# Optimization experiments

Hardware: AMD Instinct MI355X
Metric: run time of the kernel (lower is better)

Reference implementation:

```python
import jax, jax.numpy as jnp
import numpy as np

D_MODEL, D_K, D_V, N_HEADS = 1024, 64, 64, 16


def setup_inputs() -> dict:
    key = jax.random.key(0)
    ks = jax.random.split(key, 8)
    B, S = 2, 2048
    s = 0.02
    return {
        "x": jax.random.normal(ks[0], (B, S, D_MODEL), dtype=jnp.float32),
        "Wq": jax.random.normal(ks[1], (D_MODEL, N_HEADS * D_K), dtype=jnp.float32) * s,
        "bq": jnp.zeros((N_HEADS * D_K,), dtype=jnp.float32),
        "Wk": jax.random.normal(ks[2], (D_MODEL, N_HEADS * D_K), dtype=jnp.float32) * s,
        "bk": jnp.zeros((N_HEADS * D_K,), dtype=jnp.float32),
        "Wv": jax.random.normal(ks[3], (D_MODEL, N_HEADS * D_V), dtype=jnp.float32) * s,
        "bv": jnp.zeros((N_HEADS * D_V,), dtype=jnp.float32),
        "Wo": jax.random.normal(ks[4], (N_HEADS * D_V, D_MODEL), dtype=jnp.float32) * s,
    }


def reference(x, Wq, bq, Wk, bk, Wv, bv, Wo):
    B, S, _ = x.shape
    split = lambda t, d: t.reshape(B, S, N_HEADS, d).transpose(0, 2, 1, 3)  # [B,H,S,d]
    Q = split(x @ Wq + bq, D_K)
    K = split(x @ Wk + bk, D_K)
    V = split(x @ Wv + bv, D_V)
    scores = jnp.einsum("bhqd,bhkd->bhqk", Q / jnp.sqrt(jnp.float32(D_K)), K)
    # causal mask: x + (1 - 1/tril) == 0 on allowed, -inf on disallowed
    causal = jnp.tril(jnp.ones((S, S), dtype=bool))
    scores = jnp.where(causal, scores, -jnp.inf)
    attn = jax.nn.softmax(scores, axis=-1)
    out = jnp.einsum("bhqk,bhkd->bhqd", attn, V)  # [B,H,S,d_v]
    out = out.transpose(0, 2, 1, 3).reshape(B, S, N_HEADS * D_V)
    return out @ Wo
```

## Files before the change

kernel.cpp:

```cpp
#include <hip/hip_runtime.h>
#include <hip/hip_bf16.h>
#include <hip/hip_fp16.h>
#include <cstdint>

#define DEVINL __device__ __forceinline__

typedef __attribute__((ext_vector_type(4))) float floatx4;
typedef __attribute__((ext_vector_type(8))) __bf16 bf16x8;
typedef __attribute__((ext_vector_type(4))) _Float16 half4;
typedef __attribute__((ext_vector_type(8))) _Float16 half8;
typedef __attribute__((ext_vector_type(4))) unsigned short u16x4;

DEVINL floatx4 mfma_16x16x32(bf16x8 a, bf16x8 b, floatx4 c) {
  return __builtin_amdgcn_mfma_f32_16x16x32_bf16(a, b, c, 0, 0, 0);
}
DEVINL floatx4 mfma_16x16x16_f16(half4 a, half4 b, floatx4 c) {
  return __builtin_amdgcn_mfma_f32_16x16x16f16(a, b, c, 0, 0, 0);
}

DEVINL void async_copy16(const void* g, void* l) {
  __builtin_amdgcn_global_load_lds(
      (__attribute__((address_space(1))) void*)(void*)g,
      (__attribute__((address_space(3))) void*)l, 16, 0, 0);
}

#define QSCALE 0.18033688011112042f

#define VS(d, s) \
  ((d) * 128 + (((((s) >> 3)) ^ ((d) & 7)) << 4) + ((s) & 7) * 2)

__global__ void prep(const float* __restrict__ x, const float* __restrict__ Wq,
                     const float* __restrict__ Wk, const float* __restrict__ Wv,
                     const float* __restrict__ Wo,
                     __hip_bfloat16* __restrict__ xb,
                     __hip_bfloat16* __restrict__ Wt,
                     __hip_bfloat16* __restrict__ Wot) {
  const int z = blockIdx.z;
  const int tx = threadIdx.x, ty = threadIdx.y;
  if (z == 4) {
    const int bi = blockIdx.y * 32 + blockIdx.x;
    const int tid = ty * 32 + tx;
    const int base = bi * 4096 + tid * 4;
#pragma unroll
    for (int j = 0; j < 4; ++j) {
      const int i = base + j * 1024;
      const float4 v = *(const float4*)&x[i];
      xb[i + 0] = __float2bfloat16(v.x);
      xb[i + 1] = __float2bfloat16(v.y);
      xb[i + 2] = __float2bfloat16(v.z);
      xb[i + 3] = __float2bfloat16(v.w);
    }
    return;
  }
  __shared__ float tile[32][33];
  const float* W = (z == 0) ? Wq : (z == 1) ? Wk : (z == 2) ? Wv : Wo;
  __hip_bfloat16* dst = (z < 3) ? (Wt + ((int64_t)z << 20)) : Wot;
  const int k0 = blockIdx.x * 32, n0 = blockIdx.y * 32;
#pragma unroll
  for (int i = 0; i < 32; i += 8)
    tile[ty + i][tx] = W[(int64_t)(k0 + ty + i) * 1024 + n0 + tx];
  __syncthreads();
#pragma unroll
  for (int i = 0; i < 32; i += 8)
    dst[(int64_t)(n0 + ty + i) * 1024 + k0 + tx] =
        __float2bfloat16(tile[tx][ty + i]);
}

template <int MODE, int TM, int TN, int OCC>
__global__ __launch_bounds__(256, OCC) void gemm_bt(
    const __hip_bfloat16* __restrict__ A, const __hip_bfloat16* __restrict__ Bt,
    int M, int N, int K, const float* __restrict__ bq,
    const float* __restrict__ bk, const float* __restrict__ bv,
    __hip_bfloat16* __restrict__ Qb, __hip_bfloat16* __restrict__ Kb,
    _Float16* __restrict__ Vt, float* __restrict__ outf) {
  constexpr int MI = TM / 32, NJ = TN / 32;
  __shared__ __align__(16) char As[TM * 128];
  __shared__ __align__(16) char Bs[TN * 128];
  const int tid = threadIdx.x;
  const int wave = tid >> 6, lane = tid & 63;
  const int quad = lane >> 4, l16 = lane & 15;
  const int bm = blockIdx.x * TM, bn = blockIdx.y * TN;
  const int wm = (wave >> 1) * (TM / 2), wn = (wave & 1) * (TN / 2);
  const int sw = l16 & 7;

  floatx4 acc[MI][NJ] = {};

  for (int k0 = 0; k0 < K; k0 += 64) {
#pragma unroll
    for (int i = 0; i < TM / 32; ++i) {
      const int p = tid + i * 256;
      const int r = p >> 3, cc = (p & 7) ^ (r & 7);
      async_copy16(A + (int64_t)(bm + r) * K + k0 + cc * 8, As + p * 16);
    }
#pragma unroll
    for (int i = 0; i < TN / 32; ++i) {
      const int p = tid + i * 256;
      const int r = p >> 3, cc = (p & 7) ^ (r & 7);
      async_copy16(Bt + (int64_t)(bn + r) * K + k0 + cc * 8, Bs + p * 16);
    }
    __syncthreads();
    bf16x8 af[MI][2], bfr[NJ][2];
#pragma unroll
    for (int i = 0; i < MI; ++i)
#pragma unroll
      for (int h = 0; h < 2; ++h)
        af[i][h] = *(const bf16x8*)(As + (wm + i * 16 + l16) * 128 +
                                    (((h * 4 + quad) ^ sw) << 4));
#pragma unroll
    for (int j = 0; j < NJ; ++j)
#pragma unroll
      for (int h = 0; h < 2; ++h)
        bfr[j][h] = *(const bf16x8*)(Bs + (wn + j * 16 + l16) * 128 +
                                     (((h * 4 + quad) ^ sw) << 4));
#pragma unroll
    for (int i = 0; i < MI; ++i)
#pragma unroll
      for (int j = 0; j < NJ; ++j)
#pragma unroll
        for (int h = 0; h < 2; ++h)
          acc[i][j] = mfma_16x16x32(af[i][h], bfr[j][h], acc[i][j]);
    __syncthreads();
  }

  if (MODE == 1) {
#pragma unroll
    for (int i = 0; i < MI; ++i)
#pragma unroll
      for (int j = 0; j < NJ; ++j) {
        const int n = bn + wn + j * 16 + l16;
#pragma unroll
        for (int r = 0; r < 4; ++r) {
          const int m = bm + wm + i * 16 + quad * 4 + r;
          outf[(int64_t)m * N + n] = acc[i][j][r];
        }
      }
  } else if (bn < 2048) {
#pragma unroll
    for (int i = 0; i < MI; ++i)
#pragma unroll
      for (int j = 0; j < NJ; ++j) {
        const int n = bn + wn + j * 16 + l16;
        const int which = n >> 10, nn = n & 1023;
        const int h = nn >> 6, d = nn & 63;
        const float* bias = (which == 0) ? bq : bk;
#pragma unroll
        for (int r = 0; r < 4; ++r) {
          const int m = bm + wm + i * 16 + quad * 4 + r;
          const int b = m >> 11, s = m & 2047;
          float v = acc[i][j][r] + bias[nn];
          if (which == 0) v *= QSCALE;
          ((which == 0) ? Qb : Kb)[((int64_t)(b * 16 + h) * 2048 + s) * 64 + d] =
              __float2bfloat16(v);
        }
      }
  } else {
    char* scr = (wave & 1) ? Bs : As;
    const int h = ((bn + wn) & 1023) >> 6;
    const int bb = (bm + wm) >> 11;
    const int sbase = (bm + wm) & 2047;
    _Float16* dstV = Vt + (int64_t)(bb * 16 + h) * 64 * 2048;
#pragma unroll
    for (int phase = 0; phase < 2; ++phase) {
      __syncthreads();
      if ((wave >> 1) == phase) {
#pragma unroll
        for (int i = 0; i < 4; ++i)
#pragma unroll
          for (int j = 0; j < 4; ++j) {
            const int d = j * 16 + l16;
#pragma unroll
            for (int r = 0; r < 4; ++r) {
              const int s = i * 16 + quad * 4 + r;
              *(_Float16*)(scr + VS(d, s)) =
                  (_Float16)(acc[i][j][r] + bv[((bn + wn) & 1023) + d]);
            }
          }
      }
      __syncthreads();
      if ((wave >> 1) == phase) {
#pragma unroll
        for (int it = 0; it < 8; ++it) {
          const int idx = lane + it * 64;
          const int d = idx >> 3, sc = idx & 7;
          const half8 vv =
              *(const half8*)(scr + d * 128 + ((sc ^ (d & 7)) << 4));
          *(half8*)(dstV + (int64_t)d * 2048 + sbase + sc * 8) = vv;
        }
      }
    }
  }
}

__global__ __launch_bounds__(256, 3) void attn_kernel(
    const __hip_bfloat16* __restrict__ Qb, const __hip_bfloat16* __restrict__ Kb,
    const _Float16* __restrict__ Vt, __hip_bfloat16* __restrict__ Ab) {
  __shared__ __align__(16) char smem[32768];
  const int tid = threadIdx.x;
  const int wave = tid >> 6, lane = tid & 63;
  const int quad = lane >> 4, l16 = lane & 15;
  const int c = 31 - (int)(blockIdx.x >> 5);
  const int bh = blockIdx.x & 31;
  const int qbase = c * 64 + wave * 16;
  const int ktmax = c;

  const __hip_bfloat16* Qh = Qb + (int64_t)bh * 2048 * 64;
  const __hip_bfloat16* Kh = Kb + (int64_t)bh * 2048 * 64;
  const _Float16* Vh = Vt + (int64_t)bh * 64 * 2048;

  bf16x8 qf[2];
#pragma unroll
  for (int h = 0; h < 2; ++h)
    qf[h] = *(const bf16x8*)&Qh[(int64_t)(qbase + l16) * 64 + h * 32 + quad * 8];

  floatx4 o[4] = {};
  float lsum = 0.f;

  auto stage = [&](int buf, int k0s) {
#pragma unroll
    for (int i = 0; i < 2; ++i) {
      const int p = tid + i * 256;
      const int r = p >> 3, cc = (p & 7) ^ (r & 7);
      async_copy16(Kh + (int64_t)(k0s + r) * 64 + cc * 8,
                   smem + buf * 8192 + p * 16);
      async_copy16(Vh + (int64_t)r * 2048 + k0s + cc * 8,
                   smem + 16384 + buf * 8192 + p * 16);
    }
  };

  stage(0, 0);
  for (int kt = 0; kt <= ktmax; ++kt) {
    const int k0 = kt * 64;
    const int cur = kt & 1;
    __syncthreads();
    if (kt < ktmax) stage(cur ^ 1, k0 + 64);

    const char* kb = smem + cur * 8192;
    const char* vb = smem + 16384 + cur * 8192;
    const int sw = l16 & 7;

    bf16x8 kfr[4][2];
#pragma unroll
    for (int kk = 0; kk < 4; ++kk)
#pragma unroll
      for (int h = 0; h < 2; ++h)
        kfr[kk][h] = *(const bf16x8*)(kb + (kk * 16 + l16) * 128 +
                                      (((h * 4 + quad) ^ sw) << 4));

    floatx4 st[4];
#pragma unroll
    for (int kk = 0; kk < 4; ++kk) {
      floatx4 z = {};
      z = mfma_16x16x32(kfr[kk][0], qf[0], z);
      st[kk] = mfma_16x16x32(kfr[kk][1], qf[1], z);
    }

    half4 vfr[4][4];
#pragma unroll
    for (int dt = 0; dt < 4; ++dt)
#pragma unroll
      for (int kk = 0; kk < 4; ++kk)
        vfr[dt][kk] = *(const half4*)(vb + (dt * 16 + l16) * 128 +
                                      (((kk * 2 + (quad >> 1)) ^ sw) << 4) +
                                      (quad & 1) * 8);

    const bool masked = (kt == ktmax);
    half4 pf[4];
#pragma unroll
    for (int kk = 0; kk < 4; ++kk) {
#pragma unroll
      for (int r = 0; r < 4; ++r) {
        const int key = k0 + kk * 16 + quad * 4 + r;
        float p = __builtin_amdgcn_exp2f(st[kk][r]);
        if (masked && key > qbase + l16) p = 0.f;
        lsum += p;
        pf[kk][r] = (_Float16)p;
      }
    }

#pragma unroll
    for (int dt = 0; dt < 4; ++dt)
#pragma unroll
      for (int kk = 0; kk < 4; ++kk)
        o[dt] = mfma_16x16x16_f16(vfr[dt][kk], pf[kk], o[dt]);
  }

  lsum += __shfl_xor(lsum, 16, 64);
  lsum += __shfl_xor(lsum, 32, 64);
  const float invl = 1.0f / lsum;

  const int b = bh >> 4, h = bh & 15;
#pragma unroll
  for (int dt = 0; dt < 4; ++dt) {
    u16x4 pack;
#pragma unroll
    for (int r = 0; r < 4; ++r)
      pack[r] = __builtin_bit_cast(unsigned short,
                                   __float2bfloat16(o[dt][r] * invl));
    *(u16x4*)&Ab[(int64_t)(b * 2048 + qbase + l16) * 1024 + h * 64 + dt * 16 +
                 quad * 4] = pack;
  }
}

extern "C" void kernel_launch(void* const* d_in, const int* in_sizes, int n_in,
                              void* d_out, int out_size, void* d_ws,
                              size_t ws_size, hipStream_t stream) {
  const float* x = (const float*)d_in[0];
  const float* Wq = (const float*)d_in[1];
  const float* bq = (const float*)d_in[2];
  const float* Wk = (const float*)d_in[3];
  const float* bk = (const float*)d_in[4];
  const float* Wv = (const float*)d_in[5];
  const float* bv = (const float*)d_in[6];
  const float* Wo = (const float*)d_in[7];
  float* out = (float*)d_out;

  char* ws = (char*)d_ws;
  __hip_bfloat16* xb = (__hip_bfloat16*)(ws);
  __hip_bfloat16* Wt = (__hip_bfloat16*)(ws + (8ll << 20));
  __hip_bfloat16* Wot = (__hip_bfloat16*)(ws + (14ll << 20));
  __hip_bfloat16* Qb = (__hip_bfloat16*)(ws + (16ll << 20));
  __hip_bfloat16* Kb = (__hip_bfloat16*)(ws + (24ll << 20));
  _Float16* Vt = (_Float16*)(ws + (32ll << 20));
  __hip_bfloat16* Ab = xb;

  prep<<<dim3(32, 32, 5), dim3(32, 8), 0, stream>>>(x, Wq, Wk, Wv, Wo, xb, Wt,
                                                    Wot);
  gemm_bt<0, 128, 128, 3><<<dim3(32, 24), 256, 0, stream>>>(
      xb, Wt, 4096, 3072, 1024, bq, bk, bv, Qb, Kb, Vt, nullptr);
  attn_kernel<<<dim3(1024), 256, 0, stream>>>(Qb, Kb, Vt, Ab);
  gemm_bt<1, 128, 64, 2><<<dim3(32, 16), 256, 0, stream>>>(
      Ab, Wot, 4096, 1024, 1024, nullptr, nullptr, nullptr, nullptr, nullptr,
      nullptr, out);
}
```

Before: 168.8 us.

## Pair high and low causal query tiles per attention block for load balance

Each attention block now handles two query tiles, one near the end of the sequence and its mirror near the start, so every block walks the same number of key tiles and the causal triangle is evenly balanced. K/V tiles staged in shared memory are reused for both query tiles while the low tile is still active, and the grid is halved to 512 blocks. Register pressure rises from the doubled accumulators and launch bounds drop to 2 blocks per SM, which lowers occupancy. Fewer blocks also means less parallelism to hide latency.

```diff
diff --git a/kernel.cpp b/kernel.cpp
--- a/kernel.cpp
+++ b/kernel.cpp
@@ -191,29 +191,33 @@
   }
 }
 
-__global__ __launch_bounds__(256, 3) void attn_kernel(
+__global__ __launch_bounds__(256, 2) void attn_kernel(
     const __hip_bfloat16* __restrict__ Qb, const __hip_bfloat16* __restrict__ Kb,
     const _Float16* __restrict__ Vt, __hip_bfloat16* __restrict__ Ab) {
   __shared__ __align__(16) char smem[32768];
   const int tid = threadIdx.x;
   const int wave = tid >> 6, lane = tid & 63;
   const int quad = lane >> 4, l16 = lane & 15;
-  const int c = 31 - (int)(blockIdx.x >> 5);
+  const int pr = (int)(blockIdx.x >> 5);
   const int bh = blockIdx.x & 31;
-  const int qbase = c * 64 + wave * 16;
-  const int ktmax = c;
+  const int cH = 31 - pr, cL = pr;
+  const int qH = cH * 64 + wave * 16;
+  const int qL = cL * 64 + wave * 16;
+  const int ktmax = cH;
 
   const __hip_bfloat16* Qh = Qb + (int64_t)bh * 2048 * 64;
   const __hip_bfloat16* Kh = Kb + (int64_t)bh * 2048 * 64;
   const _Float16* Vh = Vt + (int64_t)bh * 64 * 2048;
 
-  bf16x8 qf[2];
-#pragma unroll
-  for (int h = 0; h < 2; ++h)
-    qf[h] = *(const bf16x8*)&Qh[(int64_t)(qbase + l16) * 64 + h * 32 + quad * 8];
-
-  floatx4 o[4] = {};
-  float lsum = 0.f;
+  bf16x8 qfH[2], qfL[2];
+#pragma unroll
+  for (int h = 0; h < 2; ++h) {
+    qfH[h] = *(const bf16x8*)&Qh[(int64_t)(qH + l16) * 64 + h * 32 + quad * 8];
+    qfL[h] = *(const bf16x8*)&Qh[(int64_t)(qL + l16) * 64 + h * 32 + quad * 8];
+  }
+
+  floatx4 oH[4] = {}, oL[4] = {};
+  float lsH = 0.f, lsL = 0.f;
 
   auto stage = [&](int buf, int k0s) {
 #pragma unroll
@@ -237,6 +241,7 @@
     const char* kb = smem + cur * 8192;
     const char* vb = smem + 16384 + cur * 8192;
     const int sw = l16 & 7;
+    const bool doL = (kt <= cL);
 
     bf16x8 kfr[4][2];
 #pragma unroll
@@ -246,12 +251,20 @@
         kfr[kk][h] = *(const bf16x8*)(kb + (kk * 16 + l16) * 128 +
                                       (((h * 4 + quad) ^ sw) << 4));
 
-    floatx4 st[4];
+    floatx4 stH[4], stL[4];
 #pragma unroll
     for (int kk = 0; kk < 4; ++kk) {
       floatx4 z = {};
-      z = mfma_16x16x32(kfr[kk][0], qf[0], z);
-      st[kk] = mfma_16x16x32(kfr[kk][1], qf[1], z);
+      z = mfma_16x16x32(kfr[kk][0], qfH[0], z);
+      stH[kk] = mfma_16x16x32(kfr[kk][1], qfH[1], z);
+    }
+    if (doL) {
+#pragma unroll
+      for (int kk = 0; kk < 4; ++kk) {
+        floatx4 z = {};
+        z = mfma_16x16x32(kfr[kk][0], qfL[0], z);
+        stL[kk] = mfma_16x16x32(kfr[kk][1], qfL[1], z);
+      }
     }
 
     half4 vfr[4][4];
@@ -263,41 +276,70 @@
                                       (((kk * 2 + (quad >> 1)) ^ sw) << 4) +
                                       (quad & 1) * 8);
 
-    const bool masked = (kt == ktmax);
-    half4 pf[4];
-#pragma unroll
-    for (int kk = 0; kk < 4; ++kk) {
-#pragma unroll
-      for (int r = 0; r < 4; ++r) {
-        const int key = k0 + kk * 16 + quad * 4 + r;
-        float p = __builtin_amdgcn_exp2f(st[kk][r]);
-        if (masked && key > qbase + l16) p = 0.f;
-        lsum += p;
-        pf[kk][r] = (_Float16)p;
-      }
-    }
-
-#pragma unroll
-    for (int dt = 0; dt < 4; ++dt)
-#pragma unroll
-      for (int kk = 0; kk < 4; ++kk)
-        o[dt] = mfma_16x16x16_f16(vfr[dt][kk], pf[kk], o[dt]);
-  }
-
-  lsum += __shfl_xor(lsum, 16, 64);
-  lsum += __shfl_xor(lsum, 32, 64);
-  const float invl = 1.0f / lsum;
+    {
+      const bool masked = (kt == cH);
+      half4 pf[4];
+#pragma unroll
+      for (int kk = 0; kk < 4; ++kk) {
+#pragma unroll
+        for (int r = 0; r < 4; ++r) {
+          const int key = k0 + kk * 16 + quad * 4 + r;
+          float p = __builtin_amdgcn_exp2f(stH[kk][r]);
+          if (masked && key > qH + l16) p = 0.f;
+          lsH += p;
+          pf[kk][r] = (_Float16)p;
+        }
+      }
+#pragma unroll
+      for (int dt = 0; dt < 4; ++dt)
+#pragma unroll
+        for (int kk = 0; kk < 4; ++kk)
+          oH[dt] = mfma_16x16x16_f16(vfr[dt][kk], pf[kk], oH[dt]);
+    }
+    if (doL) {
+      const bool masked = (kt == cL);
+      half4 pf[4];
+#pragma unroll
+      for (int kk = 0; kk < 4; ++kk) {
+#pragma unroll
+        for (int r = 0; r < 4; ++r) {
+          const int key = k0 + kk * 16 + quad * 4 + r;
+          float p = __builtin_amdgcn_exp2f(stL[kk][r]);
+          if (masked && key > qL + l16) p = 0.f;
+          lsL += p;
+          pf[kk][r] = (_Float16)p;
+        }
+      }
+#pragma unroll
+      for (int dt = 0; dt < 4; ++dt)
+#pragma unroll
+        for (int kk = 0; kk < 4; ++kk)
+          oL[dt] = mfma_16x16x16_f16(vfr[dt][kk], pf[kk], oL[dt]);
+    }
+  }
+
+  lsH += __shfl_xor(lsH, 16, 64);
+  lsH += __shfl_xor(lsH, 32, 64);
+  lsL += __shfl_xor(lsL, 16, 64);
+  lsL += __shfl_xor(lsL, 32, 64);
+  const float invH = 1.0f / lsH;
+  const float invL = 1.0f / lsL;
 
   const int b = bh >> 4, h = bh & 15;
 #pragma unroll
   for (int dt = 0; dt < 4; ++dt) {
-    u16x4 pack;
-#pragma unroll
-    for (int r = 0; r < 4; ++r)
-      pack[r] = __builtin_bit_cast(unsigned short,
-                                   __float2bfloat16(o[dt][r] * invl));
-    *(u16x4*)&Ab[(int64_t)(b * 2048 + qbase + l16) * 1024 + h * 64 + dt * 16 +
-                 quad * 4] = pack;
+    u16x4 packH, packL;
+#pragma unroll
+    for (int r = 0; r < 4; ++r) {
+      packH[r] = __builtin_bit_cast(unsigned short,
+                                    __float2bfloat16(oH[dt][r] * invH));
+      packL[r] = __builtin_bit_cast(unsigned short,
+                                    __float2bfloat16(oL[dt][r] * invL));
+    }
+    *(u16x4*)&Ab[(int64_t)(b * 2048 + qH + l16) * 1024 + h * 64 + dt * 16 +
+                 quad * 4] = packH;
+    *(u16x4*)&Ab[(int64_t)(b * 2048 + qL + l16) * 1024 + h * 64 + dt * 16 +
+                 quad * 4] = packL;
   }
 }
 
@@ -327,7 +369,7 @@
                                                     Wot);
   gemm_bt<0, 128, 128, 3><<<dim3(32, 24), 256, 0, stream>>>(
       xb, Wt, 4096, 3072, 1024, bq, bk, bv, Qb, Kb, Vt, nullptr);
-  attn_kernel<<<dim3(1024), 256, 0, stream>>>(Qb, Kb, Vt, Ab);
+  attn_kernel<<<dim3(512), 256, 0, stream>>>(Qb, Kb, Vt, Ab);
   gemm_bt<1, 128, 64, 2><<<dim3(32, 16), 256, 0, stream>>>(
       Ab, Wot, 4096, 1024, 1024, nullptr, nullptr, nullptr, nullptr, nullptr,
       nullptr, out);
```

Measured after the change: 167.7 us. No clear change (-0.7%).

## Split attention key tiles across waves with LDS cross-wave reduction

Applied to the files above, without the earlier changes.

The attention kernel stops having each wave own 16 query rows and stream every key tile through double-buffered shared memory. Each wave now handles all 64 query rows of the block for a strided subset of key tiles, reading K and V fragments straight from global memory. Partial outputs and row sums are then combined through a larger LDS buffer at the end. This is meant to drop the per-tile barriers and async staging and to balance work across waves, at the cost of more accumulator registers, lower occupancy (launch bound lowered from 3 to 2), uncoalesced global fragment loads, and an extra reduction pass.

```diff
diff --git a/kernel.cpp b/kernel.cpp
--- a/kernel.cpp
+++ b/kernel.cpp
@@ -191,113 +191,114 @@
   }
 }
 
-__global__ __launch_bounds__(256, 3) void attn_kernel(
+__global__ __launch_bounds__(256, 2) void attn_kernel(
     const __hip_bfloat16* __restrict__ Qb, const __hip_bfloat16* __restrict__ Kb,
     const _Float16* __restrict__ Vt, __hip_bfloat16* __restrict__ Ab) {
-  __shared__ __align__(16) char smem[32768];
+  __shared__ __align__(16) char smem[69632];
   const int tid = threadIdx.x;
   const int wave = tid >> 6, lane = tid & 63;
   const int quad = lane >> 4, l16 = lane & 15;
   const int c = 31 - (int)(blockIdx.x >> 5);
   const int bh = blockIdx.x & 31;
-  const int qbase = c * 64 + wave * 16;
-  const int ktmax = c;
+  const int qbase = c * 64;
 
   const __hip_bfloat16* Qh = Qb + (int64_t)bh * 2048 * 64;
   const __hip_bfloat16* Kh = Kb + (int64_t)bh * 2048 * 64;
   const _Float16* Vh = Vt + (int64_t)bh * 64 * 2048;
 
-  bf16x8 qf[2];
-#pragma unroll
-  for (int h = 0; h < 2; ++h)
-    qf[h] = *(const bf16x8*)&Qh[(int64_t)(qbase + l16) * 64 + h * 32 + quad * 8];
-
-  floatx4 o[4] = {};
-  float lsum = 0.f;
-
-  auto stage = [&](int buf, int k0s) {
-#pragma unroll
-    for (int i = 0; i < 2; ++i) {
-      const int p = tid + i * 256;
-      const int r = p >> 3, cc = (p & 7) ^ (r & 7);
-      async_copy16(Kh + (int64_t)(k0s + r) * 64 + cc * 8,
-                   smem + buf * 8192 + p * 16);
-      async_copy16(Vh + (int64_t)r * 2048 + k0s + cc * 8,
-                   smem + 16384 + buf * 8192 + p * 16);
-    }
-  };
-
-  stage(0, 0);
-  for (int kt = 0; kt <= ktmax; ++kt) {
+  bf16x8 qf[4][2];
+#pragma unroll
+  for (int qc = 0; qc < 4; ++qc)
+#pragma unroll
+    for (int h = 0; h < 2; ++h)
+      qf[qc][h] = *(const bf16x8*)&Qh[(int64_t)(qbase + qc * 16 + l16) * 64 +
+                                      h * 32 + quad * 8];
+
+  floatx4 o[4][4] = {};
+  float ls[4] = {};
+
+  for (int kt = wave; kt <= c; kt += 4) {
     const int k0 = kt * 64;
-    const int cur = kt & 1;
-    __syncthreads();
-    if (kt < ktmax) stage(cur ^ 1, k0 + 64);
-
-    const char* kb = smem + cur * 8192;
-    const char* vb = smem + 16384 + cur * 8192;
-    const int sw = l16 & 7;
-
     bf16x8 kfr[4][2];
 #pragma unroll
     for (int kk = 0; kk < 4; ++kk)
 #pragma unroll
       for (int h = 0; h < 2; ++h)
-        kfr[kk][h] = *(const bf16x8*)(kb + (kk * 16 + l16) * 128 +
-                                      (((h * 4 + quad) ^ sw) << 4));
-
-    floatx4 st[4];
-#pragma unroll
-    for (int kk = 0; kk < 4; ++kk) {
-      floatx4 z = {};
-      z = mfma_16x16x32(kfr[kk][0], qf[0], z);
-      st[kk] = mfma_16x16x32(kfr[kk][1], qf[1], z);
-    }
-
+        kfr[kk][h] = *(const bf16x8*)&Kh[(int64_t)(k0 + kk * 16 + l16) * 64 +
+                                         h * 32 + quad * 8];
     half4 vfr[4][4];
 #pragma unroll
     for (int dt = 0; dt < 4; ++dt)
 #pragma unroll
       for (int kk = 0; kk < 4; ++kk)
-        vfr[dt][kk] = *(const half4*)(vb + (dt * 16 + l16) * 128 +
-                                      (((kk * 2 + (quad >> 1)) ^ sw) << 4) +
-                                      (quad & 1) * 8);
-
-    const bool masked = (kt == ktmax);
-    half4 pf[4];
-#pragma unroll
-    for (int kk = 0; kk < 4; ++kk) {
-#pragma unroll
-      for (int r = 0; r < 4; ++r) {
-        const int key = k0 + kk * 16 + quad * 4 + r;
-        float p = __builtin_amdgcn_exp2f(st[kk][r]);
-        if (masked && key > qbase + l16) p = 0.f;
-        lsum += p;
-        pf[kk][r] = (_Float16)p;
-      }
-    }
-
+        vfr[dt][kk] = *(const half4*)&Vh[(int64_t)(dt * 16 + l16) * 2048 + k0 +
+                                         kk * 16 + quad * 4];
+
+    const bool diag = (kt == c);
+#pragma unroll
+    for (int qc = 0; qc < 4; ++qc) {
+      floatx4 st[4];
+#pragma unroll
+      for (int kk = 0; kk < 4; ++kk) {
+        floatx4 z = {};
+        z = mfma_16x16x32(kfr[kk][0], qf[qc][0], z);
+        st[kk] = mfma_16x16x32(kfr[kk][1], qf[qc][1], z);
+      }
+      half4 pf[4];
+#pragma unroll
+      for (int kk = 0; kk < 4; ++kk) {
+#pragma unroll
+        for (int r = 0; r < 4; ++r) {
+          const int key = k0 + kk * 16 + quad * 4 + r;
+          float p = __builtin_amdgcn_exp2f(st[kk][r]);
+          if (diag && key > qbase + qc * 16 + l16) p = 0.f;
+          ls[qc] += p;
+          pf[kk][r] = (_Float16)p;
+        }
+      }
+#pragma unroll
+      for (int dt = 0; dt < 4; ++dt)
+#pragma unroll
+        for (int kk = 0; kk < 4; ++kk)
+          o[dt][qc] = mfma_16x16x16_f16(vfr[dt][kk], pf[kk], o[dt][qc]);
+    }
+  }
+
+  {
+    char* ob = smem + wave * 17408;
 #pragma unroll
     for (int dt = 0; dt < 4; ++dt)
 #pragma unroll
-      for (int kk = 0; kk < 4; ++kk)
-        o[dt] = mfma_16x16x16_f16(vfr[dt][kk], pf[kk], o[dt]);
-  }
-
-  lsum += __shfl_xor(lsum, 16, 64);
-  lsum += __shfl_xor(lsum, 32, 64);
-  const float invl = 1.0f / lsum;
-
+      for (int qc = 0; qc < 4; ++qc)
+        *(floatx4*)(ob + (dt * 4 + qc) * 1024 + lane * 16) = o[dt][qc];
+    float* lsb = (float*)(ob + 16384);
+#pragma unroll
+    for (int qc = 0; qc < 4; ++qc) lsb[qc * 64 + lane] = ls[qc];
+  }
+  __syncthreads();
+
+  const int dt = wave;
   const int b = bh >> 4, h = bh & 15;
 #pragma unroll
-  for (int dt = 0; dt < 4; ++dt) {
+  for (int qc = 0; qc < 4; ++qc) {
+    floatx4 s = {};
+    float lt = 0.f;
+#pragma unroll
+    for (int w = 0; w < 4; ++w) {
+      s += *(const floatx4*)(smem + w * 17408 + (dt * 4 + qc) * 1024 +
+                             lane * 16);
+      lt += ((const float*)(smem + w * 17408 + 16384))[qc * 64 + lane];
+    }
+    lt += __shfl_xor(lt, 16, 64);
+    lt += __shfl_xor(lt, 32, 64);
+    const float inv = 1.0f / lt;
     u16x4 pack;
 #pragma unroll
     for (int r = 0; r < 4; ++r)
       pack[r] = __builtin_bit_cast(unsigned short,
-                                   __float2bfloat16(o[dt][r] * invl));
-    *(u16x4*)&Ab[(int64_t)(b * 2048 + qbase + l16) * 1024 + h * 64 + dt * 16 +
-                 quad * 4] = pack;
+                                   __float2bfloat16(s[r] * inv));
+    *(u16x4*)&Ab[(int64_t)(b * 2048 + qbase + qc * 16 + l16) * 1024 + h * 64 +
+                 dt * 16 + quad * 4] = pack;
   }
 }
 
```

Result: slower. 191.0 us (+13.1%).

## Split attention key loop across two wave groups with shared-memory reduction

Applied to the files above, without the earlier changes.

Doubles the attention block to 512 threads: two groups of four waves each process alternating 64-key tiles for the same 64 queries, each with its own double-buffered LDS region. At the end, group 1 writes its partial output and row sums to shared memory and group 0 combines them and writes the normalized result. This is meant to halve the serial key-loop length per block, which matters most for the long causal rows. In exchange it doubles LDS per block, adds a reduction step and a sync, and lowers the occupancy bound.

```diff
diff --git a/kernel.cpp b/kernel.cpp
--- a/kernel.cpp
+++ b/kernel.cpp
@@ -191,17 +191,19 @@
   }
 }
 
-__global__ __launch_bounds__(256, 3) void attn_kernel(
+__global__ __launch_bounds__(512, 2) void attn_kernel(
     const __hip_bfloat16* __restrict__ Qb, const __hip_bfloat16* __restrict__ Kb,
     const _Float16* __restrict__ Vt, __hip_bfloat16* __restrict__ Ab) {
-  __shared__ __align__(16) char smem[32768];
+  __shared__ __align__(16) char smem[65536];
   const int tid = threadIdx.x;
   const int wave = tid >> 6, lane = tid & 63;
+  const int g = wave >> 2;
+  const int w4 = wave & 3;
+  const int gtid = w4 * 64 + lane;
   const int quad = lane >> 4, l16 = lane & 15;
   const int c = 31 - (int)(blockIdx.x >> 5);
   const int bh = blockIdx.x & 31;
-  const int qbase = c * 64 + wave * 16;
-  const int ktmax = c;
+  const int qbase = c * 64 + w4 * 16;
 
   const __hip_bfloat16* Qh = Qb + (int64_t)bh * 2048 * 64;
   const __hip_bfloat16* Kh = Kb + (int64_t)bh * 2048 * 64;
@@ -215,89 +217,108 @@
   floatx4 o[4] = {};
   float lsum = 0.f;
 
+  char* const gb = smem + g * 32768;
+
   auto stage = [&](int buf, int k0s) {
 #pragma unroll
     for (int i = 0; i < 2; ++i) {
-      const int p = tid + i * 256;
+      const int p = gtid + i * 256;
       const int r = p >> 3, cc = (p & 7) ^ (r & 7);
       async_copy16(Kh + (int64_t)(k0s + r) * 64 + cc * 8,
-                   smem + buf * 8192 + p * 16);
+                   gb + buf * 16384 + p * 16);
       async_copy16(Vh + (int64_t)r * 2048 + k0s + cc * 8,
-                   smem + 16384 + buf * 8192 + p * 16);
+                   gb + buf * 16384 + 8192 + p * 16);
     }
   };
 
-  stage(0, 0);
-  for (int kt = 0; kt <= ktmax; ++kt) {
-    const int k0 = kt * 64;
-    const int cur = kt & 1;
+  const int NT = (c >> 1) + 1;
+  if (g <= c) stage(0, g * 64);
+
+  for (int t = 0; t < NT; ++t) {
+    const int kt = 2 * t + g;
+    const bool active = (kt <= c);
     __syncthreads();
-    if (kt < ktmax) stage(cur ^ 1, k0 + 64);
-
-    const char* kb = smem + cur * 8192;
-    const char* vb = smem + 16384 + cur * 8192;
-    const int sw = l16 & 7;
-
-    bf16x8 kfr[4][2];
-#pragma unroll
-    for (int kk = 0; kk < 4; ++kk)
-#pragma unroll
-      for (int h = 0; h < 2; ++h)
-        kfr[kk][h] = *(const bf16x8*)(kb + (kk * 16 + l16) * 128 +
-                                      (((h * 4 + quad) ^ sw) << 4));
-
-    floatx4 st[4];
-#pragma unroll
-    for (int kk = 0; kk < 4; ++kk) {
-      floatx4 z = {};
-      z = mfma_16x16x32(kfr[kk][0], qf[0], z);
-      st[kk] = mfma_16x16x32(kfr[kk][1], qf[1], z);
-    }
-
-    half4 vfr[4][4];
+    if (active && kt + 2 <= c) stage((t + 1) & 1, (kt + 2) * 64);
+    if (active) {
+      const int k0 = kt * 64;
+      const char* kb = gb + (t & 1) * 16384;
+      const char* vb = kb + 8192;
+      const int sw = l16 & 7;
+
+      bf16x8 kfr[4][2];
+#pragma unroll
+      for (int kk = 0; kk < 4; ++kk)
+#pragma unroll
+        for (int h = 0; h < 2; ++h)
+          kfr[kk][h] = *(const bf16x8*)(kb + (kk * 16 + l16) * 128 +
+                                        (((h * 4 + quad) ^ sw) << 4));
+
+      floatx4 st[4];
+#pragma unroll
+      for (int kk = 0; kk < 4; ++kk) {
+        floatx4 z = {};
+        z = mfma_16x16x32(kfr[kk][0], qf[0], z);
+        st[kk] = mfma_16x16x32(kfr[kk][1], qf[1], z);
+      }
+
+      half4 vfr[4][4];
+#pragma unroll
+      for (int dt = 0; dt < 4; ++dt)
+#pragma unroll
+        for (int kk = 0; kk < 4; ++kk)
+          vfr[dt][kk] = *(const half4*)(vb + (dt * 16 + l16) * 128 +
+                                        (((kk * 2 + (quad >> 1)) ^ sw) << 4) +
+                                        (quad & 1) * 8);
+
+      const bool masked = (kt == c);
+      half4 pf[4];
+#pragma unroll
+      for (int kk = 0; kk < 4; ++kk) {
+#pragma unroll
+        for (int r = 0; r < 4; ++r) {
+          const int key = k0 + kk * 16 + quad * 4 + r;
+          float p = __builtin_amdgcn_exp2f(st[kk][r]);
+          if (masked && key > qbase + l16) p = 0.f;
+          lsum += p;
+          pf[kk][r] = (_Float16)p;
+        }
+      }
+
+#pragma unroll
+      for (int dt = 0; dt < 4; ++dt)
+#pragma unroll
+        for (int kk = 0; kk < 4; ++kk)
+          o[dt] = mfma_16x16x16_f16(vfr[dt][kk], pf[kk], o[dt]);
+    }
+  }
+
+  __syncthreads();
+  if (g == 1) {
+    char* ob = smem + w4 * 4352;
 #pragma unroll
     for (int dt = 0; dt < 4; ++dt)
-#pragma unroll
-      for (int kk = 0; kk < 4; ++kk)
-        vfr[dt][kk] = *(const half4*)(vb + (dt * 16 + l16) * 128 +
-                                      (((kk * 2 + (quad >> 1)) ^ sw) << 4) +
-                                      (quad & 1) * 8);
-
-    const bool masked = (kt == ktmax);
-    half4 pf[4];
-#pragma unroll
-    for (int kk = 0; kk < 4; ++kk) {
-#pragma unroll
-      for (int r = 0; r < 4; ++r) {
-        const int key = k0 + kk * 16 + quad * 4 + r;
-        float p = __builtin_amdgcn_exp2f(st[kk][r]);
-        if (masked && key > qbase + l16) p = 0.f;
-        lsum += p;
-        pf[kk][r] = (_Float16)p;
-      }
-    }
-
-#pragma unroll
-    for (int dt = 0; dt < 4; ++dt)
-#pragma unroll
-      for (int kk = 0; kk < 4; ++kk)
-        o[dt] = mfma_16x16x16_f16(vfr[dt][kk], pf[kk], o[dt]);
-  }
-
-  lsum += __shfl_xor(lsum, 16, 64);
-  lsum += __shfl_xor(lsum, 32, 64);
-  const float invl = 1.0f / lsum;
-
-  const int b = bh >> 4, h = bh & 15;
-#pragma unroll
-  for (int dt = 0; dt < 4; ++dt) {
-    u16x4 pack;
-#pragma unroll
-    for (int r = 0; r < 4; ++r)
-      pack[r] = __builtin_bit_cast(unsigned short,
-                                   __float2bfloat16(o[dt][r] * invl));
-    *(u16x4*)&Ab[(int64_t)(b * 2048 + qbase + l16) * 1024 + h * 64 + dt * 16 +
-                 quad * 4] = pack;
+      *(floatx4*)(ob + dt * 1024 + lane * 16) = o[dt];
+    ((float*)(ob + 4096))[lane] = lsum;
+  }
+  __syncthreads();
+  if (g == 0) {
+    const char* pb = smem + w4 * 4352;
+    float lt = lsum + ((const float*)(pb + 4096))[lane];
+    lt += __shfl_xor(lt, 16, 64);
+    lt += __shfl_xor(lt, 32, 64);
+    const float inv = 1.0f / lt;
+    const int b = bh >> 4, h = bh & 15;
+#pragma unroll
+    for (int dt = 0; dt < 4; ++dt) {
+      const floatx4 s = o[dt] + *(const floatx4*)(pb + dt * 1024 + lane * 16);
+      u16x4 pack;
+#pragma unroll
+      for (int r = 0; r < 4; ++r)
+        pack[r] = __builtin_bit_cast(unsigned short,
+                                     __float2bfloat16(s[r] * inv));
+      *(u16x4*)&Ab[(int64_t)(b * 2048 + qbase + l16) * 1024 + h * 64 +
+                   dt * 16 + quad * 4] = pack;
+    }
   }
 }
 
@@ -327,7 +348,7 @@
                                                     Wot);
   gemm_bt<0, 128, 128, 3><<<dim3(32, 24), 256, 0, stream>>>(
       xb, Wt, 4096, 3072, 1024, bq, bk, bv, Qb, Kb, Vt, nullptr);
-  attn_kernel<<<dim3(1024), 256, 0, stream>>>(Qb, Kb, Vt, Ab);
+  attn_kernel<<<dim3(1024), 512, 0, stream>>>(Qb, Kb, Vt, Ab);
   gemm_bt<1, 128, 64, 2><<<dim3(32, 16), 256, 0, stream>>>(
       Ab, Wot, 4096, 1024, 1024, nullptr, nullptr, nullptr, nullptr, nullptr,
       nullptr, out);
```

Result: slower. 173.7 us (+2.9%).
